# Performance work log

Hardware: AMD Instinct MI355X
Metric: run time of the kernel (lower is better)

The kernel has to match this reference:

```python
import jax, jax.numpy as jnp
import numpy as np

KSIZE = 5
# OpenCV: sigma=0 -> sigma = 0.3*((ksize-1)*0.5 - 1) + 0.8
SIGMA = 0.3 * ((KSIZE - 1) * 0.5 - 1.0) + 0.8  # = 1.1 for ksize=5


def _gauss_taps(ksize, sigma):
    r = (ksize - 1) / 2.0
    xs = np.arange(ksize, dtype=np.float64) - r
    w = np.exp(-(xs ** 2) / (2.0 * sigma ** 2))
    w /= w.sum()
    return jnp.asarray(w, dtype=jnp.float32)


def setup_inputs() -> dict:
    key = jax.random.key(0)
    x = jax.random.normal(key, (64, 384, 512, 3), dtype=jnp.float32)
    return {"x": x}


def reference(x):
    # Separable 5x5 Gaussian blur, OpenCV default border BORDER_REFLECT_101
    # (numpy/jnp 'reflect' mode, edge pixel not repeated).
    w = _gauss_taps(KSIZE, SIGMA)  # [5]
    pad = KSIZE // 2
    B, H, W, C = x.shape
    # vertical pass
    xp = jnp.pad(x, ((0, 0), (pad, pad), (0, 0), (0, 0)), mode="reflect")
    y = sum(w[k] * xp[:, k:k + H, :, :] for k in range(KSIZE))
    # horizontal pass
    yp = jnp.pad(y, ((0, 0), (0, 0), (pad, pad), (0, 0)), mode="reflect")
    out = sum(w[k] * yp[:, :, k:k + W, :] for k in range(KSIZE))
    return out
```

## Files before the change

### kernel.cpp

```cpp
#include <hip/hip_runtime.h>


#define BN 64
#define HN 384
#define WN 512
#define CN 3
#define ROWF (WN * CN)
#define ROWQ (ROWF / 4)
#define TH 4
#define NTILES (HN / TH)
#define NT 384
#define NBLK (BN * NTILES)

#define PADQ 2
#define LROWQ (ROWQ + 2 * PADQ)
#define LROWF (LROWQ * 4)

#define CW0 0.07076630f
#define CW1 0.24446040f
#define CW2 0.36954650f

typedef float vfloat4 __attribute__((ext_vector_type(4)));

__global__ __launch_bounds__(NT, 6) void gauss_blur_fused(
        const float* __restrict__ x, float* __restrict__ out) {
    __shared__ float v[TH * LROWF];

    const int bid  = blockIdx.x;
    const int tile = (bid & 7) * (NBLK >> 3) + (bid >> 3);
    const int b    = tile / NTILES;
    const int h0   = (tile - b * NTILES) * TH;
    const float* __restrict__ xb = x + (size_t)b * HN * ROWF;
    float* __restrict__ ob = out + (size_t)b * HN * ROWF + (size_t)h0 * ROWF;

    const int q = threadIdx.x;

    float4 rowv[TH + 4];
#pragma unroll
    for (int i = 0; i < TH + 4; ++i) {
        int hs = h0 + i - 2;
        hs = hs < 0 ? -hs : hs;
        hs = hs >= HN ? 2 * HN - 2 - hs : hs;
        rowv[i] = ((const float4*)(xb + (size_t)hs * ROWF))[q];
    }
#pragma unroll
    for (int r = 0; r < TH; ++r) {
        float4 a;
        a.x = CW0 * (rowv[r].x + rowv[r + 4].x) +
              CW1 * (rowv[r + 1].x + rowv[r + 3].x) + CW2 * rowv[r + 2].x;
        a.y = CW0 * (rowv[r].y + rowv[r + 4].y) +
              CW1 * (rowv[r + 1].y + rowv[r + 3].y) + CW2 * rowv[r + 2].y;
        a.z = CW0 * (rowv[r].z + rowv[r + 4].z) +
              CW1 * (rowv[r + 1].z + rowv[r + 3].z) + CW2 * rowv[r + 2].z;
        a.w = CW0 * (rowv[r].w + rowv[r + 4].w) +
              CW1 * (rowv[r + 1].w + rowv[r + 3].w) + CW2 * rowv[r + 2].w;
        ((float4*)(v + r * LROWF))[PADQ + q] = a;
    }
    __syncthreads();

    if (threadIdx.x < TH * 12) {
        int r = threadIdx.x / 12;
        int p = threadIdx.x - r * 12;
        float* vr = v + r * LROWF + 4 * PADQ;
        int dst, src;
        if (p < 6) {
            dst = p - 6;
            src = (p < 3) ? 6 + p : p;
        } else {
            int pp = p - 6;
            dst = 1536 + pp;
            src = (pp < 3) ? 1530 + pp : 1524 + pp;
        }
        vr[dst] = vr[src];
    }
    __syncthreads();

#pragma unroll
    for (int r = 0; r < TH; ++r) {
        const float* vr = v + r * LROWF;
        float wnd[20];
#pragma unroll
        for (int j = 0; j < 5; ++j) {
            float4 t = ((const float4*)vr)[q + j];
            wnd[4 * j + 0] = t.x;
            wnd[4 * j + 1] = t.y;
            wnd[4 * j + 2] = t.z;
            wnd[4 * j + 3] = t.w;
        }
        vfloat4 res;
#pragma unroll
        for (int j = 0; j < 4; ++j) {
            res[j] =
                CW0 * (wnd[j + 2] + wnd[j + 14]) +
                CW1 * (wnd[j + 5] + wnd[j + 11]) +
                CW2 * wnd[j + 8];
        }
        __builtin_nontemporal_store(res, &((vfloat4*)ob)[r * ROWQ + q]);
    }
}

extern "C" void kernel_launch(void* const* d_in, const int* in_sizes, int n_in,
                              void* d_out, int out_size, void* d_ws, size_t ws_size,
                              hipStream_t stream) {
    const float* x = (const float*)d_in[0];
    float* out = (float*)d_out;
    gauss_blur_fused<<<dim3(NBLK), dim3(NT), 0, stream>>>(x, out);
}
```

Before: 257.8 us.

## Process 24-row strips per block with rolling row window and prefetch

Each block now handles a strip of 24 rows in 6 iterations of 4, keeping a rolling 8-row register window so vertical halo rows are loaded once per strip instead of being reloaded for every 4-row tile. The next 4 input rows are prefetched before the current rows are computed, overlapping loads with compute. The separate halo-fill pass and one barrier are replaced by edge threads writing the reflected border values directly. Fewer blocks are launched and each now runs more serial iterations with two barriers per iteration, which may reduce latency hiding.

```diff
diff --git a/kernel.cpp b/kernel.cpp
--- a/kernel.cpp
+++ b/kernel.cpp
@@ -8,9 +8,11 @@
 #define ROWF (WN * CN)
 #define ROWQ (ROWF / 4)
 #define TH 4
-#define NTILES (HN / TH)
+#define SROWS 24
+#define NITER (SROWS / TH)
+#define NSTRIP (HN / SROWS)
 #define NT 384
-#define NBLK (BN * NTILES)
+#define NBLK (BN * NSTRIP)
 
 #define PADQ 2
 #define LROWQ (ROWQ + 2 * PADQ)
@@ -28,74 +30,90 @@
 
     const int bid  = blockIdx.x;
     const int tile = (bid & 7) * (NBLK >> 3) + (bid >> 3);
-    const int b    = tile / NTILES;
-    const int h0   = (tile - b * NTILES) * TH;
+    const int b    = tile / NSTRIP;
+    const int h0   = (tile - b * NSTRIP) * SROWS;
     const float* __restrict__ xb = x + (size_t)b * HN * ROWF;
-    float* __restrict__ ob = out + (size_t)b * HN * ROWF + (size_t)h0 * ROWF;
+    float* __restrict__ ob = out + (size_t)b * HN * ROWF;
 
     const int q = threadIdx.x;
 
-    float4 rowv[TH + 4];
+    float4 win[TH + 4];
 #pragma unroll
     for (int i = 0; i < TH + 4; ++i) {
         int hs = h0 + i - 2;
         hs = hs < 0 ? -hs : hs;
-        hs = hs >= HN ? 2 * HN - 2 - hs : hs;
-        rowv[i] = ((const float4*)(xb + (size_t)hs * ROWF))[q];
+        win[i] = ((const float4*)(xb + (size_t)hs * ROWF))[q];
     }
+
+    for (int t = 0; t < NITER; ++t) {
+        const int r0 = h0 + t * TH;
+
+        float4 nxt[TH];
+        if (t + 1 < NITER) {
+            const int rb = r0 + TH + 2;
 #pragma unroll
-    for (int r = 0; r < TH; ++r) {
-        float4 a;
-        a.x = CW0 * (rowv[r].x + rowv[r + 4].x) +
-              CW1 * (rowv[r + 1].x + rowv[r + 3].x) + CW2 * rowv[r + 2].x;
-        a.y = CW0 * (rowv[r].y + rowv[r + 4].y) +
-              CW1 * (rowv[r + 1].y + rowv[r + 3].y) + CW2 * rowv[r + 2].y;
-        a.z = CW0 * (rowv[r].z + rowv[r + 4].z) +
-              CW1 * (rowv[r + 1].z + rowv[r + 3].z) + CW2 * rowv[r + 2].z;
-        a.w = CW0 * (rowv[r].w + rowv[r + 4].w) +
-              CW1 * (rowv[r + 1].w + rowv[r + 3].w) + CW2 * rowv[r + 2].w;
-        ((float4*)(v + r * LROWF))[PADQ + q] = a;
-    }
-    __syncthreads();
-
-    if (threadIdx.x < TH * 12) {
-        int r = threadIdx.x / 12;
-        int p = threadIdx.x - r * 12;
-        float* vr = v + r * LROWF + 4 * PADQ;
-        int dst, src;
-        if (p < 6) {
-            dst = p - 6;
-            src = (p < 3) ? 6 + p : p;
-        } else {
-            int pp = p - 6;
-            dst = 1536 + pp;
-            src = (pp < 3) ? 1530 + pp : 1524 + pp;
+            for (int i = 0; i < TH; ++i) {
+                int hs = rb + i;
+                hs = hs >= HN ? 2 * HN - 2 - hs : hs;
+                nxt[i] = ((const float4*)(xb + (size_t)hs * ROWF))[q];
+            }
         }
-        vr[dst] = vr[src];
-    }
-    __syncthreads();
 
 #pragma unroll
-    for (int r = 0; r < TH; ++r) {
-        const float* vr = v + r * LROWF;
-        float wnd[20];
+        for (int r = 0; r < TH; ++r) {
+            float4 a;
+            a.x = CW0 * (win[r].x + win[r + 4].x) +
+                  CW1 * (win[r + 1].x + win[r + 3].x) + CW2 * win[r + 2].x;
+            a.y = CW0 * (win[r].y + win[r + 4].y) +
+                  CW1 * (win[r + 1].y + win[r + 3].y) + CW2 * win[r + 2].y;
+            a.z = CW0 * (win[r].z + win[r + 4].z) +
+                  CW1 * (win[r + 1].z + win[r + 3].z) + CW2 * win[r + 2].z;
+            a.w = CW0 * (win[r].w + win[r + 4].w) +
+                  CW1 * (win[r + 1].w + win[r + 3].w) + CW2 * win[r + 2].w;
+            float* vr = v + r * LROWF + 4 * PADQ;
+            ((float4*)vr)[q] = a;
+            if (q == 0)        { vr[-3] = a.w; }
+            else if (q == 1)   { vr[-2] = a.x; vr[-1] = a.y;
+                                 vr[-6] = a.z; vr[-5] = a.w; }
+            else if (q == 2)   { vr[-4] = a.x; }
+            else if (q == 381) { vr[1539] = a.w; }
+            else if (q == 382) { vr[1540] = a.x; vr[1541] = a.y;
+                                 vr[1536] = a.z; vr[1537] = a.w; }
+            else if (q == 383) { vr[1538] = a.x; }
+        }
+
 #pragma unroll
-        for (int j = 0; j < 5; ++j) {
-            float4 t = ((const float4*)vr)[q + j];
-            wnd[4 * j + 0] = t.x;
-            wnd[4 * j + 1] = t.y;
-            wnd[4 * j + 2] = t.z;
-            wnd[4 * j + 3] = t.w;
+        for (int i = 0; i < TH; ++i) win[i] = win[i + 4];
+#pragma unroll
+        for (int i = 0; i < TH; ++i) win[TH + i] = nxt[i];
+
+        __syncthreads();
+
+#pragma unroll
+        for (int r = 0; r < TH; ++r) {
+            const float* vr = v + r * LROWF;
+            float wnd[20];
+#pragma unroll
+            for (int j = 0; j < 5; ++j) {
+                float4 tq = ((const float4*)vr)[q + j];
+                wnd[4 * j + 0] = tq.x;
+                wnd[4 * j + 1] = tq.y;
+                wnd[4 * j + 2] = tq.z;
+                wnd[4 * j + 3] = tq.w;
+            }
+            vfloat4 res;
+#pragma unroll
+            for (int j = 0; j < 4; ++j) {
+                res[j] =
+                    CW0 * (wnd[j + 2] + wnd[j + 14]) +
+                    CW1 * (wnd[j + 5] + wnd[j + 11]) +
+                    CW2 * wnd[j + 8];
+            }
+            __builtin_nontemporal_store(res,
+                &((vfloat4*)ob)[(size_t)(r0 + r) * ROWQ + q]);
         }
-        vfloat4 res;
-#pragma unroll
-        for (int j = 0; j < 4; ++j) {
-            res[j] =
-                CW0 * (wnd[j + 2] + wnd[j + 14]) +
-                CW1 * (wnd[j + 5] + wnd[j + 11]) +
-                CW2 * wnd[j + 8];
-        }
-        __builtin_nontemporal_store(res, &((vfloat4*)ob)[r * ROWQ + q]);
+
+        __syncthreads();
     }
 }
 
```

Result: slower. 276.1 us (+7.1%).

## Split row tile into per-wave column strips with halos to drop block barriers

Applied to the files above, without the earlier changes.

Each 64-lane wave now owns a 48-quad column strip and also loads a 2-quad halo on each side from global memory. It keeps its own LDS slice and fixes the left and right reflect borders inside the boundary waves. This removes both block-wide __syncthreads and the shared border-fixup step, relying on in-wave ordering of LDS accesses. The cost is about a third more global loads, though the overlap should mostly hit in cache, plus 16 idle lanes per wave in the horizontal pass. The block also grows to 512 threads.

```diff
diff --git a/kernel.cpp b/kernel.cpp
--- a/kernel.cpp
+++ b/kernel.cpp
@@ -9,12 +9,8 @@
 #define ROWQ (ROWF / 4)
 #define TH 4
 #define NTILES (HN / TH)
-#define NT 384
+#define NTHR 512
 #define NBLK (BN * NTILES)
-
-#define PADQ 2
-#define LROWQ (ROWQ + 2 * PADQ)
-#define LROWF (LROWQ * 4)
 
 #define CW0 0.07076630f
 #define CW1 0.24446040f
@@ -22,80 +18,82 @@
 
 typedef float vfloat4 __attribute__((ext_vector_type(4)));
 
-__global__ __launch_bounds__(NT, 6) void gauss_blur_fused(
+__global__ __launch_bounds__(NTHR, 6) void gauss_blur_fused(
         const float* __restrict__ x, float* __restrict__ out) {
-    __shared__ float v[TH * LROWF];
+    __shared__ float v[8 * 4 * 256];
 
     const int bid  = blockIdx.x;
     const int tile = (bid & 7) * (NBLK >> 3) + (bid >> 3);
     const int b    = tile / NTILES;
     const int h0   = (tile - b * NTILES) * TH;
     const float* __restrict__ xb = x + (size_t)b * HN * ROWF;
-    float* __restrict__ ob = out + (size_t)b * HN * ROWF + (size_t)h0 * ROWF;
+    float* __restrict__ ob = out + ((size_t)b * HN + h0) * ROWF;
 
-    const int q = threadIdx.x;
+    const int wid = threadIdx.x >> 6;
+    const int l   = threadIdx.x & 63;
+    const int q0  = wid * 48;
+    int c = q0 - 2 + l;
+    c = c < 0 ? 0 : (c > ROWQ - 1 ? ROWQ - 1 : c);
 
-    float4 rowv[TH + 4];
+    float4 win[8];
 #pragma unroll
-    for (int i = 0; i < TH + 4; ++i) {
+    for (int i = 0; i < 8; ++i) {
         int hs = h0 + i - 2;
         hs = hs < 0 ? -hs : hs;
         hs = hs >= HN ? 2 * HN - 2 - hs : hs;
-        rowv[i] = ((const float4*)(xb + (size_t)hs * ROWF))[q];
+        win[i] = ((const float4*)(xb + (size_t)hs * ROWF))[c];
     }
+
+    float* const vw = v + wid * (TH * 256);
+
 #pragma unroll
     for (int r = 0; r < TH; ++r) {
         float4 a;
-        a.x = CW0 * (rowv[r].x + rowv[r + 4].x) +
-              CW1 * (rowv[r + 1].x + rowv[r + 3].x) + CW2 * rowv[r + 2].x;
-        a.y = CW0 * (rowv[r].y + rowv[r + 4].y) +
-              CW1 * (rowv[r + 1].y + rowv[r + 3].y) + CW2 * rowv[r + 2].y;
-        a.z = CW0 * (rowv[r].z + rowv[r + 4].z) +
-              CW1 * (rowv[r + 1].z + rowv[r + 3].z) + CW2 * rowv[r + 2].z;
-        a.w = CW0 * (rowv[r].w + rowv[r + 4].w) +
-              CW1 * (rowv[r + 1].w + rowv[r + 3].w) + CW2 * rowv[r + 2].w;
-        ((float4*)(v + r * LROWF))[PADQ + q] = a;
+        a.x = CW0 * (win[r].x + win[r + 4].x) +
+              CW1 * (win[r + 1].x + win[r + 3].x) + CW2 * win[r + 2].x;
+        a.y = CW0 * (win[r].y + win[r + 4].y) +
+              CW1 * (win[r + 1].y + win[r + 3].y) + CW2 * win[r + 2].y;
+        a.z = CW0 * (win[r].z + win[r + 4].z) +
+              CW1 * (win[r + 1].z + win[r + 3].z) + CW2 * win[r + 2].z;
+        a.w = CW0 * (win[r].w + win[r + 4].w) +
+              CW1 * (win[r + 1].w + win[r + 3].w) + CW2 * win[r + 2].w;
+        ((float4*)(vw + r * 256))[l] = a;
     }
-    __syncthreads();
 
-    if (threadIdx.x < TH * 12) {
-        int r = threadIdx.x / 12;
-        int p = threadIdx.x - r * 12;
-        float* vr = v + r * LROWF + 4 * PADQ;
-        int dst, src;
-        if (p < 6) {
-            dst = p - 6;
-            src = (p < 3) ? 6 + p : p;
-        } else {
-            int pp = p - 6;
-            dst = 1536 + pp;
-            src = (pp < 3) ? 1530 + pp : 1524 + pp;
+    if (q0 == 0 && l < TH * 6) {
+        int r = l / 6, p = l - 6 * r;
+        float* vr = vw + r * 256;
+        vr[2 + p] = vr[p < 3 ? 14 + p : 8 + p];
+    } else if (q0 == 336 && l < TH * 6) {
+        int r = l / 6, p = l - 6 * r;
+        float* vr = vw + r * 256;
+        vr[200 + p] = vr[p < 3 ? 194 + p : 188 + p];
+    }
+
+    if (l < 48) {
+#pragma unroll
+        for (int r = 0; r < TH; ++r) {
+            const float* vr = vw + r * 256;
+            float wnd[20];
+#pragma unroll
+            for (int k = 0; k < 5; ++k) {
+                float4 t = ((const float4*)vr)[l + k];
+                wnd[4 * k + 0] = t.x;
+                wnd[4 * k + 1] = t.y;
+                wnd[4 * k + 2] = t.z;
+                wnd[4 * k + 3] = t.w;
+            }
+            vfloat4 res;
+#pragma unroll
+            for (int j = 0; j < 4; ++j) {
+                res[j] =
+                    CW0 * (wnd[j + 2] + wnd[j + 14]) +
+                    CW1 * (wnd[j + 5] + wnd[j + 11]) +
+                    CW2 * wnd[j + 8];
+            }
+            __builtin_nontemporal_store(res,
+                &((vfloat4*)ob)[r * ROWQ + q0 + l]);
         }
-        vr[dst] = vr[src];
-    }
-    __syncthreads();
-
-#pragma unroll
-    for (int r = 0; r < TH; ++r) {
-        const float* vr = v + r * LROWF;
-        float wnd[20];
-#pragma unroll
-        for (int j = 0; j < 5; ++j) {
-            float4 t = ((const float4*)vr)[q + j];
-            wnd[4 * j + 0] = t.x;
-            wnd[4 * j + 1] = t.y;
-            wnd[4 * j + 2] = t.z;
-            wnd[4 * j + 3] = t.w;
-        }
-        vfloat4 res;
-#pragma unroll
-        for (int j = 0; j < 4; ++j) {
-            res[j] =
-                CW0 * (wnd[j + 2] + wnd[j + 14]) +
-                CW1 * (wnd[j + 5] + wnd[j + 11]) +
-                CW2 * wnd[j + 8];
-        }
-        __builtin_nontemporal_store(res, &((vfloat4*)ob)[r * ROWQ + q]);
     }
 }
 
@@ -104,5 +102,5 @@
                               hipStream_t stream) {
     const float* x = (const float*)d_in[0];
     float* out = (float*)d_out;
-    gauss_blur_fused<<<dim3(NBLK), dim3(NT), 0, stream>>>(x, out);
+    gauss_blur_fused<<<dim3(NBLK), dim3(NTHR), 0, stream>>>(x, out);
 }
```

New measurement: 258.6 us. Within noise of the previous version (+0.3%).
